# Optimization experiments

Hardware: AMD Instinct MI355X
Metric: run time of the kernel (lower is better)

Reference implementation:

```python
import jax, jax.numpy as jnp
import numpy as np
import math

B, S, D = 4, 2048, 1024
E, DFF = 8, 4096
CAP_FACTOR, MIN_CAP = 1.25, 4


def setup_inputs() -> dict:
    key = jax.random.key(0)
    ks = jax.random.split(key, 6)
    inputs = jax.random.normal(ks[0], (B, S, D), dtype=jnp.float32)
    gate_weight = jax.random.normal(ks[1], (E, D), dtype=jnp.float32) * math.sqrt(0.1 / D)
    w1 = jax.random.normal(ks[2], (E, D, DFF), dtype=jnp.float32) * 0.02
    b1 = jax.random.normal(ks[3], (E, DFF), dtype=jnp.float32) * 0.01
    w2 = jax.random.normal(ks[4], (E, DFF, D), dtype=jnp.float32) * 0.02
    b2 = jax.random.normal(ks[5], (E, D), dtype=jnp.float32) * 0.01
    return {"inputs": inputs, "gate_weight": gate_weight, "w1": w1, "b1": b1, "w2": w2, "b2": b2}


def _capacity(num_tokens: int, num_experts: int) -> int:
    cap = int(CAP_FACTOR * num_tokens / num_experts)
    cap += cap % 2  # ColossalAI rounds capacity up to even
    return max(cap, MIN_CAP)


def reference(inputs, gate_weight, w1, b1, w2, b2):
    d_model = inputs.shape[-1]
    tokens = inputs.reshape(-1, d_model)                      # [T, D]
    T = tokens.shape[0]
    num_experts = gate_weight.shape[0]
    cap = _capacity(T, num_experts)

    # gating in fp32 (F.linear(fp32_input, fp32_weight))
    logits = tokens.astype(jnp.float32) @ gate_weight.astype(jnp.float32).T  # [T, E]
    probs = jax.nn.softmax(logits, axis=-1)

    # Top-1 routing
    top1_idx = jnp.argmax(logits, axis=-1)                    # [T]
    mask = jax.nn.one_hot(top1_idx, num_experts, dtype=jnp.int32)  # [T, E]

    # auxiliary load-balance loss
    me = probs.mean(axis=0)
    ce = mask.astype(jnp.float32).mean(axis=0)
    l_aux = num_experts * jnp.sum(me * ce)

    # capacity-limited ranks (moe_cumsum = cumsum - 1 along tokens)
    ranks = jnp.cumsum(mask, axis=0) - 1                      # [T, E]
    mask = mask * (ranks < cap).astype(jnp.int32)
    rank1 = jnp.sum(mask * ranks, axis=-1)                    # [T]
    ranks_oh = jax.nn.one_hot(rank1, cap, dtype=probs.dtype)  # [T, C]

    weight = mask.astype(probs.dtype) * probs                 # [T, E]
    combine_weights = weight[:, :, None] * ranks_oh[:, None, :]  # [T, E, C]
    sec_mask_f = (combine_weights != 0).astype(tokens.dtype)     # [T, E, C]

    # dispatch: mask-matmul scatter of tokens into expert slots
    dispatch = jnp.einsum('tec,td->ecd', sec_mask_f, tokens)  # [E, C, D]

    # per-expert FFN (ep_size = 1, so AllToAll is identity)
    h = jax.nn.gelu(jnp.einsum('ecd,edf->ecf', dispatch, w1) + b1[:, None, :])
    expert_out = jnp.einsum('ecf,efd->ecd', h, w2) + b2[:, None, :]  # [E, C, D]

    # combine: weighted gather back to tokens
    ans = combine_weights.reshape(T, -1) @ expert_out.reshape(-1, d_model)
    return ans.reshape(inputs.shape), l_aux
```

## Files before the change

### kernel.cpp

```cpp
#include <hip/hip_runtime.h>


#define TKN    8192
#define DMODEL 1024
#define NEXP   8
#define DFFN   4096
#define CAPC   1280

typedef __attribute__((ext_vector_type(8))) short short8;
typedef __attribute__((ext_vector_type(4))) float f32x4;

__device__ __forceinline__ unsigned short f2bf(float f) {
  unsigned int u = __float_as_uint(f);
  u += 0x7fffu + ((u >> 16) & 1u);
  return (unsigned short)(u >> 16);
}
__device__ __forceinline__ float gelu_tanh(float x) {
  const float c0 = 0.7978845608028654f;
  const float c1 = 0.044715f;
  float inner = c0 * (x + c1 * x * x * x);
  return 0.5f * x * (1.0f + tanhf(inner));
}
__device__ __forceinline__ void gload_lds16(const void* g, void* l) {
  __builtin_amdgcn_global_load_lds(
      (const __attribute__((address_space(1))) void*)g,
      (__attribute__((address_space(3))) void*)l, 16, 0, 0);
}

__global__ __launch_bounds__(256) void k_init(int* __restrict__ slot_token,
                                              float* __restrict__ me_sum) {
  int i = blockIdx.x * 256 + threadIdx.x;
  if (i < NEXP * CAPC) slot_token[i] = -1;
  if (i < NEXP) me_sum[i] = 0.0f;
}

__global__ __launch_bounds__(256) void k_gate(const float* __restrict__ x,
                                              const float* __restrict__ gw,
                                              int* __restrict__ top1,
                                              float* __restrict__ p1,
                                              float* __restrict__ me_sum) {
  const int wave = threadIdx.x >> 6;
  const int lane = threadIdx.x & 63;
  const int t = blockIdx.x * 4 + wave;
  const float* xrow = x + (size_t)t * DMODEL;

  float acc[NEXP] = {};
  for (int k = lane; k < DMODEL; k += 64) {
    float xv = xrow[k];
#pragma unroll
    for (int e = 0; e < NEXP; ++e) acc[e] = fmaf(xv, gw[e * DMODEL + k], acc[e]);
  }
#pragma unroll
  for (int e = 0; e < NEXP; ++e) {
    float v = acc[e];
    v += __shfl_xor(v, 32); v += __shfl_xor(v, 16); v += __shfl_xor(v, 8);
    v += __shfl_xor(v, 4);  v += __shfl_xor(v, 2);  v += __shfl_xor(v, 1);
    acc[e] = v;
  }
  float m = acc[0];
  int idx = 0;
#pragma unroll
  for (int e = 1; e < NEXP; ++e) {
    if (acc[e] > m) { m = acc[e]; idx = e; }
  }
  float pe[NEXP];
  float s = 0.0f;
#pragma unroll
  for (int e = 0; e < NEXP; ++e) { pe[e] = expf(acc[e] - m); s += pe[e]; }
  float inv = 1.0f / s;

  __shared__ float lme[4][NEXP];
  if (lane == 0) {
#pragma unroll
    for (int e = 0; e < NEXP; ++e) lme[wave][e] = pe[e] * inv;
    top1[t] = idx;
    p1[t] = inv;
  }
  __syncthreads();
  if (threadIdx.x < NEXP) {
    float v = lme[0][threadIdx.x] + lme[1][threadIdx.x] + lme[2][threadIdx.x] + lme[3][threadIdx.x];
    atomicAdd(&me_sum[threadIdx.x], v);
  }
}

__global__ __launch_bounds__(1024) void k_scan(const int* __restrict__ top1,
                                               const float* __restrict__ me_sum,
                                               int* __restrict__ rankk,
                                               float* __restrict__ out_laux) {
  __shared__ int base[NEXP];
  __shared__ int wcnt[16][NEXP];
  const int tid = threadIdx.x;
  const int w = tid >> 6, lane = tid & 63;
  if (tid < NEXP) base[tid] = 0;
  __syncthreads();

  for (int r = 0; r < TKN; r += 1024) {
    int e = top1[r + tid];
    int myrank = 0;
#pragma unroll
    for (int ee = 0; ee < NEXP; ++ee) {
      unsigned long long b = __ballot(e == ee);
      if (ee == e) myrank = __popcll(b & ((1ull << lane) - 1ull));
      if (lane == 0) wcnt[w][ee] = __popcll(b);
    }
    __syncthreads();
    int pre = base[e];
    for (int ww = 0; ww < w; ++ww) pre += wcnt[ww][e];
    int rank = pre + myrank;
    rankk[r + tid] = (rank < CAPC) ? rank : -1;
    __syncthreads();
    if (tid < NEXP) {
      int s = 0;
#pragma unroll
      for (int ww = 0; ww < 16; ++ww) s += wcnt[ww][tid];
      base[tid] += s;
    }
    __syncthreads();
  }

  if (tid == 0) {
    float s = 0.0f;
    for (int e = 0; e < NEXP; ++e) {
      float me = me_sum[e] * (1.0f / (float)TKN);
      float ce = (float)base[e] * (1.0f / (float)TKN);
      s += me * ce;
    }
    *out_laux = (float)NEXP * s;
  }
}

__global__ __launch_bounds__(256) void k_dispatch(const float* __restrict__ x,
                                                  const int* __restrict__ top1,
                                                  const int* __restrict__ rankk,
                                                  int* __restrict__ slot_token,
                                                  unsigned short* __restrict__ Xb,
                                                  float* __restrict__ out) {
  const int t = blockIdx.x;
  const int tid = threadIdx.x;
  const int r = rankk[t];
  if (r < 0) {
    float4 z = {0.f, 0.f, 0.f, 0.f};
    *(float4*)(out + (size_t)t * DMODEL + tid * 4) = z;
    return;
  }
  const int e = top1[t];
  const int slot = e * CAPC + r;
  if (tid == 0) slot_token[slot] = t;
  float4 v = *(const float4*)(x + (size_t)t * DMODEL + tid * 4);
  ushort4 h;
  h.x = f2bf(v.x); h.y = f2bf(v.y); h.z = f2bf(v.z); h.w = f2bf(v.w);
  *(ushort4*)(Xb + (size_t)slot * DMODEL + tid * 4) = h;
}

__global__ __launch_bounds__(256) void k_wtrans(const float* __restrict__ W,
                                                unsigned short* __restrict__ WT,
                                                int K, int N, int k_off, int Kt,
                                                int n_off, int Nt) {
  __shared__ float ls[32][33];
  const int e = blockIdx.z, kt = blockIdx.y, nt = blockIdx.x;
  const int t = threadIdx.x;
  {
    const int kl = t >> 3, nl0 = (t & 7) * 4;
    const float* src = W + (size_t)e * K * N + (size_t)(k_off + kt * 32 + kl) * N + n_off + nt * 32 + nl0;
    float4 v = *(const float4*)src;
    ls[kl][nl0 + 0] = v.x; ls[kl][nl0 + 1] = v.y;
    ls[kl][nl0 + 2] = v.z; ls[kl][nl0 + 3] = v.w;
  }
  __syncthreads();
  {
    const int nl = t >> 3, kl0 = (t & 7) * 4;
    ushort4 o;
    o.x = f2bf(ls[kl0 + 0][nl]); o.y = f2bf(ls[kl0 + 1][nl]);
    o.z = f2bf(ls[kl0 + 2][nl]); o.w = f2bf(ls[kl0 + 3][nl]);
    *(ushort4*)(WT + (size_t)e * Nt * Kt + (size_t)(nt * 32 + nl) * Kt + kt * 32 + kl0) = o;
  }
}

template <int MODE>
__global__ __launch_bounds__(256) void k_gemm(
    const unsigned short* __restrict__ A, int lda,
    const unsigned short* __restrict__ Bm, int ldb,
    int nK,
    const float* __restrict__ bias, int bias_off, int bias_ld,
    unsigned short* __restrict__ Hout, int ldh,
    const int* __restrict__ slot_token,
    const float* __restrict__ p1,
    float* __restrict__ out) {
  __shared__ __align__(16) unsigned short As[128 * 64];
  __shared__ __align__(16) unsigned short Bs[128 * 64];
  const int e = blockIdx.z, mt = blockIdx.y, nt = blockIdx.x;
  const int tid = threadIdx.x;
  const int w = tid >> 6, lane = tid & 63;
  const int wr = w >> 1, wc = w & 1;
  const int N = gridDim.x * 128;

  const unsigned short* Abase = A + (size_t)(e * CAPC + mt * 128) * lda;
  const unsigned short* Bbase = Bm + (size_t)e * N * ldb + (size_t)(nt * 128) * ldb;

  const int srow = w * 32 + (lane >> 3);
  const int scol = (lane & 7) * 8;
  unsigned short* ldsA = &As[(w * 32) * 64];
  unsigned short* ldsB = &Bs[(w * 32) * 64];

  f32x4 acc[4][4];
#pragma unroll
  for (int m = 0; m < 4; ++m)
#pragma unroll
    for (int n = 0; n < 4; ++n) acc[m][n] = (f32x4){0.f, 0.f, 0.f, 0.f};

  const int arow = wr * 64 + (lane & 15);
  const int brow = wc * 64 + (lane & 15);
  const int kcol = (lane >> 4) * 8;

  for (int t = 0; t < nK; ++t) {
    const size_t k0 = (size_t)t * 64;
#pragma unroll
    for (int j = 0; j < 4; ++j)
      gload_lds16(Abase + (size_t)(srow + j * 8) * lda + k0 + scol, ldsA + j * 8 * 64);
#pragma unroll
    for (int j = 0; j < 4; ++j)
      gload_lds16(Bbase + (size_t)(srow + j * 8) * ldb + k0 + scol, ldsB + j * 8 * 64);
    __syncthreads();
#pragma unroll
    for (int kk = 0; kk < 64; kk += 32) {
      short8 av[4], bv[4];
#pragma unroll
      for (int m = 0; m < 4; ++m) av[m] = *(const short8*)&As[(arow + m * 16) * 64 + kk + kcol];
#pragma unroll
      for (int n = 0; n < 4; ++n) bv[n] = *(const short8*)&Bs[(brow + n * 16) * 64 + kk + kcol];
#pragma unroll
      for (int m = 0; m < 4; ++m)
#pragma unroll
        for (int n = 0; n < 4; ++n)
          acc[m][n] = __builtin_amdgcn_mfma_f32_16x16x32_bf16(av[m], bv[n], acc[m][n], 0, 0, 0);
    }
    __syncthreads();
  }

  const int colf = lane & 15;
  const int rsub = (lane >> 4) * 4;
#pragma unroll
  for (int m = 0; m < 4; ++m) {
#pragma unroll
    for (int i = 0; i < 4; ++i) {
      const int slot_l = mt * 128 + wr * 64 + m * 16 + rsub + i;
      if (MODE == 0) {
        const size_t hrow = ((size_t)(e * CAPC) + slot_l) * ldh;
#pragma unroll
        for (int n = 0; n < 4; ++n) {
          const int col = nt * 128 + wc * 64 + n * 16 + colf;
          float v = acc[m][n][i] + bias[e * bias_ld + bias_off + col];
          Hout[hrow + col] = f2bf(gelu_tanh(v));
        }
      } else {
        const int slotg = e * CAPC + slot_l;
        const int tkn = slot_token[slotg];
        if (tkn >= 0) {
          const float p = p1[tkn];
#pragma unroll
          for (int n = 0; n < 4; ++n) {
            const int col = nt * 128 + wc * 64 + n * 16 + colf;
            float v = acc[m][n][i];
            if (MODE == 2) v += bias[e * bias_ld + col];
            float o = p * v;
            float* dst = out + (size_t)tkn * DMODEL + col;
            if (MODE == 2) *dst = *dst + o;
            else *dst = o;
          }
        }
      }
    }
  }
}

extern "C" void kernel_launch(void* const* d_in, const int* in_sizes, int n_in,
                              void* d_out, int out_size, void* d_ws, size_t ws_size,
                              hipStream_t stream) {
  const float* x  = (const float*)d_in[0];
  const float* gw = (const float*)d_in[1];
  const float* w1 = (const float*)d_in[2];
  const float* b1 = (const float*)d_in[3];
  const float* w2 = (const float*)d_in[4];
  const float* b2 = (const float*)d_in[5];
  float* out = (float*)d_out;

  char* ws = (char*)d_ws;
  float* me_sum     = (float*)(ws + 0);
  int*   top1       = (int*)(ws + 1024);
  float* p1         = (float*)(ws + 33792);
  int*   rankk      = (int*)(ws + 66560);
  int*   slot_token = (int*)(ws + 99328);
  unsigned short* Xb = (unsigned short*)(ws + 140288);
  unsigned short* H  = (unsigned short*)(ws + 21111808);
  unsigned short* WB = (unsigned short*)(ws + 63054848);

  k_init<<<40, 256, 0, stream>>>(slot_token, me_sum);
  k_gate<<<TKN / 4, 256, 0, stream>>>(x, gw, top1, p1, me_sum);
  k_scan<<<1, 1024, 0, stream>>>(top1, me_sum, rankk, out + (size_t)TKN * DMODEL);
  k_dispatch<<<TKN, 256, 0, stream>>>(x, top1, rankk, slot_token, Xb, out);

  k_wtrans<<<dim3(64, 32, NEXP), 256, 0, stream>>>(w1, WB, DMODEL, DFFN, 0, DMODEL, 0, 2048);
  k_gemm<0><<<dim3(16, 10, NEXP), 256, 0, stream>>>(Xb, DMODEL, WB, DMODEL, DMODEL / 64,
                                                    b1, 0, DFFN, H, 2048,
                                                    nullptr, nullptr, nullptr);
  k_wtrans<<<dim3(32, 64, NEXP), 256, 0, stream>>>(w2, WB, DFFN, DMODEL, 0, 2048, 0, DMODEL);
  k_gemm<1><<<dim3(8, 10, NEXP), 256, 0, stream>>>(H, 2048, WB, 2048, 2048 / 64,
                                                   b2, 0, DMODEL, nullptr, 0,
                                                   slot_token, p1, out);

  k_wtrans<<<dim3(64, 32, NEXP), 256, 0, stream>>>(w1, WB, DMODEL, DFFN, 0, DMODEL, 2048, 2048);
  k_gemm<0><<<dim3(16, 10, NEXP), 256, 0, stream>>>(Xb, DMODEL, WB, DMODEL, DMODEL / 64,
                                                    b1, 2048, DFFN, H, 2048,
                                                    nullptr, nullptr, nullptr);
  k_wtrans<<<dim3(32, 64, NEXP), 256, 0, stream>>>(w2, WB, DFFN, DMODEL, 2048, 2048, 0, DMODEL);
  k_gemm<2><<<dim3(8, 10, NEXP), 256, 0, stream>>>(H, 2048, WB, 2048, 2048 / 64,
                                                   b2, 0, DMODEL, nullptr, 0,
                                                   slot_token, p1, out);
}
```

Before: 787.6 us.

## Double-buffer GEMM LDS tiles and XOR-swizzle layout to avoid bank conflicts

The bf16 MFMA GEMM now keeps two LDS buffers for the A and B tiles. The next K-tile's global-to-LDS loads are issued before computing on the current tile, with explicit vmcnt waits and barriers, so memory latency overlaps with MFMA work. The LDS column chunk is also XOR-swizzled by row, which should reduce bank conflicts on the short8 fragment reads. In exchange, LDS use per block doubles to 64KB, which may lower occupancy, and correctness now depends on the hand-written waitcnt counts.

```diff
diff --git a/kernel.cpp b/kernel.cpp
--- a/kernel.cpp
+++ b/kernel.cpp
@@ -186,8 +186,8 @@
     const int* __restrict__ slot_token,
     const float* __restrict__ p1,
     float* __restrict__ out) {
-  __shared__ __align__(16) unsigned short As[128 * 64];
-  __shared__ __align__(16) unsigned short Bs[128 * 64];
+  __shared__ __align__(16) unsigned short As[2][128 * 64];
+  __shared__ __align__(16) unsigned short Bs[2][128 * 64];
   const int e = blockIdx.z, mt = blockIdx.y, nt = blockIdx.x;
   const int tid = threadIdx.x;
   const int w = tid >> 6, lane = tid & 63;
@@ -197,10 +197,8 @@
   const unsigned short* Abase = A + (size_t)(e * CAPC + mt * 128) * lda;
   const unsigned short* Bbase = Bm + (size_t)e * N * ldb + (size_t)(nt * 128) * ldb;
 
-  const int srow = w * 32 + (lane >> 3);
-  const int scol = (lane & 7) * 8;
-  unsigned short* ldsA = &As[(w * 32) * 64];
-  unsigned short* ldsB = &Bs[(w * 32) * 64];
+  const int srow_base = w * 32 + (lane >> 3);
+  const int sslot = (lane & 7) ^ (lane >> 3);
 
   f32x4 acc[4][4];
 #pragma unroll
@@ -210,32 +208,54 @@
 
   const int arow = wr * 64 + (lane & 15);
   const int brow = wc * 64 + (lane & 15);
-  const int kcol = (lane >> 4) * 8;
-
+  const int hi = lane >> 4;
+  const int rm = lane & 7;
+
+#define STAGE_TILE(buf, t)                                                              \
+  do {                                                                                  \
+    const size_t k0s = (size_t)(t) * 64 + (size_t)sslot * 8;                            \
+    _Pragma("unroll") for (int j = 0; j < 4; ++j)                                       \
+        gload_lds16(Abase + (size_t)(srow_base + j * 8) * lda + k0s,                    \
+                    &As[buf][(w * 32 + j * 8) * 64]);                                   \
+    _Pragma("unroll") for (int j = 0; j < 4; ++j)                                       \
+        gload_lds16(Bbase + (size_t)(srow_base + j * 8) * ldb + k0s,                    \
+                    &Bs[buf][(w * 32 + j * 8) * 64]);                                   \
+  } while (0)
+
+  STAGE_TILE(0, 0);
   for (int t = 0; t < nK; ++t) {
-    const size_t k0 = (size_t)t * 64;
-#pragma unroll
-    for (int j = 0; j < 4; ++j)
-      gload_lds16(Abase + (size_t)(srow + j * 8) * lda + k0 + scol, ldsA + j * 8 * 64);
-#pragma unroll
-    for (int j = 0; j < 4; ++j)
-      gload_lds16(Bbase + (size_t)(srow + j * 8) * ldb + k0 + scol, ldsB + j * 8 * 64);
-    __syncthreads();
+    const int cur = t & 1;
+    if (t + 1 < nK) {
+      STAGE_TILE(cur ^ 1, t + 1);
+      asm volatile("s_waitcnt vmcnt(8)" ::: "memory");
+    } else {
+      asm volatile("s_waitcnt vmcnt(0)" ::: "memory");
+    }
+    __builtin_amdgcn_sched_barrier(0);
+    __builtin_amdgcn_s_barrier();
+
 #pragma unroll
     for (int kk = 0; kk < 64; kk += 32) {
+      const int sb = (kk >> 3) + hi;
       short8 av[4], bv[4];
 #pragma unroll
-      for (int m = 0; m < 4; ++m) av[m] = *(const short8*)&As[(arow + m * 16) * 64 + kk + kcol];
-#pragma unroll
-      for (int n = 0; n < 4; ++n) bv[n] = *(const short8*)&Bs[(brow + n * 16) * 64 + kk + kcol];
+      for (int m = 0; m < 4; ++m)
+        av[m] = *(const short8*)&As[cur][(arow + m * 16) * 64 + ((sb ^ rm) << 3)];
+#pragma unroll
+      for (int n = 0; n < 4; ++n)
+        bv[n] = *(const short8*)&Bs[cur][(brow + n * 16) * 64 + ((sb ^ rm) << 3)];
 #pragma unroll
       for (int m = 0; m < 4; ++m)
 #pragma unroll
         for (int n = 0; n < 4; ++n)
           acc[m][n] = __builtin_amdgcn_mfma_f32_16x16x32_bf16(av[m], bv[n], acc[m][n], 0, 0, 0);
     }
-    __syncthreads();
-  }
+
+    asm volatile("s_waitcnt lgkmcnt(0)" ::: "memory");
+    __builtin_amdgcn_sched_barrier(0);
+    __builtin_amdgcn_s_barrier();
+  }
+#undef STAGE_TILE
 
   const int colf = lane & 15;
   const int rsub = (lane >> 4) * 4;
```

After: 722.3 us. 8.3% less time.
